# Optimization experiments

Hardware: AMD Instinct MI355X
Metric: run time of the kernel (lower is better)

Reference implementation:

```python
import jax, jax.numpy as jnp
import numpy as np

PRIOR = 0.2
TEMP = 1.0
THRESHOLD = 0.5
B, L, D, H = 8, 4096, 768, 512


def setup_inputs() -> dict:
    key = jax.random.key(0)
    k1, k2, k3, k4 = jax.random.split(key, 4)
    hidden = jax.random.normal(k1, (B, L, D), jnp.float32)
    # MLP params: Linear(D,H) -> ReLU -> Linear(H,1)
    W1 = jax.random.normal(k2, (D, H), jnp.float32) / np.sqrt(D).astype(np.float32)
    b1 = jnp.zeros((H,), jnp.float32)
    W2 = jax.random.normal(k3, (H, 1), jnp.float32) / np.sqrt(H).astype(np.float32)
    b2 = jnp.zeros((1,), jnp.float32)
    # pre-sampled uniform noise for the RelaxedBernoulli logistic reparameterization
    noise_u = jax.random.uniform(k4, (B, L), jnp.float32, minval=1e-6, maxval=1.0 - 1e-6)
    return dict(hidden=hidden, W1=W1, b1=b1, W2=W2, b2=b2, noise_u=noise_u)


def reference(hidden, W1, b1, W2, b2, noise_u):
    bs, seq_len, model_dim = hidden.shape
    # boundary MLP -> per-token logits [B, L]
    h = jax.nn.relu(jnp.einsum('bld,dh->blh', hidden, W1) + b1)
    logits = (jnp.einsum('blh,ho->blo', h, W2) + b2)[..., 0]
    # RelaxedBernoulli rsample: sigmoid((logits + logistic_noise) / temp),
    # since logit(sigmoid(logits)) == logits
    logistic_noise = jnp.log(noise_u) - jnp.log1p(-noise_u)
    soft_boundaries = jax.nn.sigmoid((logits + logistic_noise) / TEMP)
    hard_bin = (soft_boundaries > THRESHOLD).astype(soft_boundaries.dtype)
    # straight-through estimator
    hard_boundaries = soft_boundaries + jax.lax.stop_gradient(hard_bin - soft_boundaries)
    # segment id of each token: number of boundaries strictly before it
    # (boundary token is the last element of its segment)
    seg = (jnp.cumsum(hard_bin, axis=1) - hard_bin).astype(jnp.int32)  # [B, L] in [0, L)
    ids = (seg + seq_len * jnp.arange(bs, dtype=jnp.int32)[:, None]).reshape(-1)
    flat = hidden.reshape(bs * seq_len, model_dim)
    seg_sum = jax.ops.segment_sum(flat, ids, num_segments=bs * seq_len)
    seg_cnt = jax.ops.segment_sum(jnp.ones((bs * seq_len,), hidden.dtype), ids,
                                  num_segments=bs * seq_len)
    # mean pooling per segment; unused segment slots stay zero (padded to L segments,
    # equivalent to the torch [S,B,D]->transpose output up to zero padding)
    pooled = (seg_sum / jnp.maximum(seg_cnt, 1.0)[:, None]).reshape(bs, seq_len, model_dim)
    # hinge loss on boundary rate: penalize |rate - (prior+0.05)| beyond margin 0.05
    ratio = jnp.mean(hard_boundaries)
    loss = jax.nn.relu(jnp.abs(ratio - (PRIOR + 0.05)) - 0.05)
    num_boundaries = jnp.sum(hard_bin)
    total_positions = jnp.asarray(bs * seq_len, jnp.float32)
    return pooled, loss, num_boundaries, total_positions
```

## Files before the change

kernel.cpp:

```cpp
#include <hip/hip_runtime.h>
#include <math.h>

typedef __attribute__((ext_vector_type(8))) short short8;
typedef __attribute__((ext_vector_type(4))) float float4v;
typedef unsigned int uint;

#define BATCH 8
#define SEQ   4096
#define DIM   768
#define HID   512
#define M_TOK (BATCH * SEQ)

static __device__ __forceinline__ short f2bf_rne(float x) {
    unsigned int u = __float_as_uint(x);
    unsigned int r = (u + 0x7FFFu + ((u >> 16) & 1u)) >> 16;
    return (short)r;
}
static __device__ __forceinline__ uint pack_bf2(float a, float b) {
    return __builtin_amdgcn_perm(__float_as_uint(b), __float_as_uint(a), 0x07060302u);
}
union FragU { uint u[4]; short8 s; };

__global__ __launch_bounds__(256) void prep_kernel(const float* __restrict__ W1,
                                                   short* __restrict__ W1T) {
    int idx = blockIdx.x * 256 + threadIdx.x;
    if (idx < DIM * HID) {
        int k = idx / HID, n = idx % HID;
        W1T[n * DIM + k] = f2bf_rne(W1[idx]);
    }
}

__global__ __launch_bounds__(256) void mlp_kernel(const float* __restrict__ A,
                                                  const short* __restrict__ BT,
                                                  const float* __restrict__ b1,
                                                  const float* __restrict__ W2,
                                                  float* __restrict__ partial) {
    __shared__ short As[2][64 * 72];

    const int m0 = blockIdx.x * 64;
    const int tid = threadIdx.x;
    const int wave = tid >> 6, lane = tid & 63;
    const int quad = lane >> 4, r = lane & 15;
    const int srow = tid >> 2, scol = (tid & 3) * 16;
    const float* aPtr = A + (size_t)(m0 + srow) * DIM + scol;
    const int lw = srow * 72 + scol;
    const short* bPtr = BT + (size_t)(wave * 128 + r) * DIM + quad * 8;

    float4v s[4];
    short8  bfr[2][8];
#pragma unroll
    for (int i = 0; i < 4; i++) s[i] = *(const float4v*)(aPtr + i * 4);
#pragma unroll
    for (int j = 0; j < 8; j++) bfr[0][j] = *(const short8*)(bPtr + j * 16 * DIM);
    {
        uint pk[8];
#pragma unroll
        for (int i = 0; i < 4; i++) {
            pk[2 * i]     = pack_bf2(s[i][0], s[i][1]);
            pk[2 * i + 1] = pack_bf2(s[i][2], s[i][3]);
        }
        *(short8*)(&As[0][lw])     = *(short8*)&pk[0];
        *(short8*)(&As[0][lw + 8]) = *(short8*)&pk[4];
    }
    float4v acc[4][8] = {};
    __syncthreads();

    int ks = 0;
#pragma unroll
    for (int p = 0; p < 12; ++p) {
        const int cur = p & 1;
        if (p < 11) {
            const float* ap = aPtr + (p + 1) * 64;
#pragma unroll
            for (int i = 0; i < 4; i++) s[i] = *(const float4v*)(ap + i * 4);
        }
#pragma unroll
        for (int h = 0; h < 2; ++h, ++ks) {
            const int bb = ks & 1;
            if (ks < 23) {
                const short* bp = bPtr + (ks + 1) * 32;
#pragma unroll
                for (int j = 0; j < 8; j++)
                    bfr[bb ^ 1][j] = *(const short8*)(bp + j * 16 * DIM);
            }
            FragU af[4];
#pragma unroll
            for (int mf = 0; mf < 4; mf++)
                af[mf].s = *(const short8*)(&As[cur][(mf * 16 + r) * 72 + h * 32 + quad * 8]);
#pragma unroll
            for (int mf = 0; mf < 4; mf++)
#pragma unroll
                for (int j = 0; j < 8; j++)
                    acc[mf][j] = __builtin_amdgcn_mfma_f32_16x16x32_bf16(
                        af[mf].s, bfr[bb][j], acc[mf][j], 0, 0, 0);
        }
        if (p < 11) {
            uint pk[8];
#pragma unroll
            for (int i = 0; i < 4; i++) {
                pk[2 * i]     = pack_bf2(s[i][0], s[i][1]);
                pk[2 * i + 1] = pack_bf2(s[i][2], s[i][3]);
            }
            *(short8*)(&As[cur ^ 1][lw])     = *(short8*)&pk[0];
            *(short8*)(&As[cur ^ 1][lw + 8]) = *(short8*)&pk[4];
        }
        __syncthreads();
    }

    float b1v[8], w2v[8];
#pragma unroll
    for (int j = 0; j < 8; j++) {
        int gc = wave * 128 + j * 16 + r;
        b1v[j] = b1[gc];
        w2v[j] = W2[gc];
    }
#pragma unroll
    for (int mf = 0; mf < 4; mf++)
#pragma unroll
        for (int v = 0; v < 4; v++) {
            float pp = 0.f;
#pragma unroll
            for (int j = 0; j < 8; j++) {
                float hh = acc[mf][j][v] + b1v[j];
                hh = hh > 0.f ? hh : 0.f;
                pp += hh * w2v[j];
            }
#pragma unroll
            for (int off = 1; off < 16; off <<= 1) pp += __shfl_xor(pp, off, 64);
            if (r == 0)
                partial[(size_t)wave * M_TOK + m0 + mf * 16 + quad * 4 + v] = pp;
        }
}

__global__ __launch_bounds__(1024) void boundary_kernel(const float* __restrict__ partial,
                                                        const float* __restrict__ b2p,
                                                        const float* __restrict__ noise,
                                                        int* __restrict__ starts,
                                                        int* __restrict__ nseg,
                                                        int* __restrict__ nbcount) {
    const int b = blockIdx.x, tid = threadIdx.x;
    const int base = tid * 4;
    const float b2 = b2p[0];
    int h[4], c = 0;
#pragma unroll
    for (int j = 0; j < 4; j++) {
        int l = base + j;
        float u = noise[b * SEQ + l];
        float nz = logf(u) - log1pf(-u);
        float lg = b2 + nz;
#pragma unroll
        for (int q = 0; q < 4; q++) lg += partial[(size_t)q * M_TOK + b * SEQ + l];
        h[j] = (lg > 0.f) ? 1 : 0;
        c += h[j];
    }
    const int lane = tid & 63, wid = tid >> 6;
    int inc = c;
    for (int off = 1; off < 64; off <<= 1) {
        int t = __shfl_up(inc, off, 64);
        if (lane >= off) inc += t;
    }
    __shared__ int wtot[16], woff[16], extra[2];
    if (lane == 63) wtot[wid] = inc;
    if (tid == 1023) extra[0] = h[3];
    __syncthreads();
    if (tid == 0) {
        int s = 0;
        for (int i = 0; i < 16; i++) { woff[i] = s; s += wtot[i]; }
        extra[1] = s;
    }
    __syncthreads();
    int run = (inc - c) + woff[wid];
#pragma unroll
    for (int j = 0; j < 4; j++) {
        int l = base + j;
        if (h[j]) {
            run++;
            if (l < SEQ - 1) starts[b * (SEQ + 1) + run] = l + 1;
        }
    }
    if (tid == 0) {
        int total = extra[1];
        int ns = total + (extra[0] ? 0 : 1);
        starts[b * (SEQ + 1)] = 0;
        starts[b * (SEQ + 1) + ns] = SEQ;
        nseg[b] = ns;
        nbcount[b] = total;
    }
}

__global__ __launch_bounds__(256) void pool_kernel(const float* __restrict__ hidden,
                                                   const int* __restrict__ starts,
                                                   const int* __restrict__ nseg,
                                                   float* __restrict__ out) {
    const int wid = threadIdx.x >> 6, lane = threadIdx.x & 63;
    const int s = blockIdx.x * 4 + wid, b = blockIdx.y;
    float* orow = out + (size_t)(b * SEQ + s) * DIM;
    const int ns = nseg[b];
    if (s >= ns) {
        float4v z = {0.f, 0.f, 0.f, 0.f};
        *(float4v*)(orow + lane * 4)         = z;
        *(float4v*)(orow + (lane + 64) * 4)  = z;
        *(float4v*)(orow + (lane + 128) * 4) = z;
        return;
    }
    const int st = starts[b * (SEQ + 1) + s];
    const int en = starts[b * (SEQ + 1) + s + 1];
    float4v a0 = {0.f, 0.f, 0.f, 0.f}, a1 = a0, a2 = a0;
    const float* hbase = hidden + (size_t)(b * SEQ) * DIM;
    for (int row = st; row < en; row++) {
        const float* hr = hbase + (size_t)row * DIM;
        a0 += *(const float4v*)(hr + lane * 4);
        a1 += *(const float4v*)(hr + (lane + 64) * 4);
        a2 += *(const float4v*)(hr + (lane + 128) * 4);
    }
    const float invc = 1.f / (float)(en - st);
    a0 *= invc; a1 *= invc; a2 *= invc;
    *(float4v*)(orow + lane * 4)         = a0;
    *(float4v*)(orow + (lane + 64) * 4)  = a1;
    *(float4v*)(orow + (lane + 128) * 4) = a2;
}

__global__ void finalize_kernel(const int* __restrict__ nbcount, float* __restrict__ tail) {
    int nb = 0;
    for (int i = 0; i < BATCH; i++) nb += nbcount[i];
    float ratio = (float)nb / (float)M_TOK;
    float d = fabsf(ratio - 0.25f) - 0.05f;
    tail[0] = d > 0.f ? d : 0.f;
    tail[1] = (float)nb;
    tail[2] = (float)M_TOK;
}

extern "C" void kernel_launch(void* const* d_in, const int* in_sizes, int n_in,
                              void* d_out, int out_size, void* d_ws, size_t ws_size,
                              hipStream_t stream) {
    const float* hidden = (const float*)d_in[0];
    const float* W1     = (const float*)d_in[1];
    const float* b1     = (const float*)d_in[2];
    const float* W2     = (const float*)d_in[3];
    const float* b2     = (const float*)d_in[4];
    const float* noise  = (const float*)d_in[5];

    char* ws = (char*)d_ws;
    short* W1T     = (short*)(ws);
    float* partial = (float*)(ws + 786432);
    int*   starts  = (int*)(ws + 1310720);
    int*   nseg    = (int*)(ws + 1441824);
    int*   nbcount = nseg + 8;
    float* out     = (float*)d_out;

    prep_kernel<<<1536, 256, 0, stream>>>(W1, W1T);
    mlp_kernel<<<512, 256, 0, stream>>>(hidden, W1T, b1, W2, partial);
    boundary_kernel<<<BATCH, 1024, 0, stream>>>(partial, b2, noise, starts, nseg, nbcount);
    pool_kernel<<<dim3(SEQ / 4, BATCH), 256, 0, stream>>>(hidden, starts, nseg, out);
    finalize_kernel<<<1, 1, 0, stream>>>(nbcount, out + (size_t)M_TOK * DIM);
}
```

Measured before the change: 263.5 us.

## Stage GEMM operands via direct global-to-LDS loads and tile W1 transpose

The MLP GEMM now loads fp32 activations and bf16 weights straight into LDS with global_load_lds, using an XOR swizzle, and converts A to bf16 at fragment-read time instead of holding register-prefetched fragments. The four per-wave partial logits are reduced in shared memory, so one logits array is written instead of four. The W1 transpose uses a shared-memory tiled kernel with coalesced writes. The pool kernel unrolls its row loop by two and uses nontemporal stores. The GEMM loses its register double buffering and now syncs twice per 32-wide k-step, which could expose load latency.

```diff
diff --git a/kernel.cpp b/kernel.cpp
--- a/kernel.cpp
+++ b/kernel.cpp
@@ -20,119 +20,129 @@
     return __builtin_amdgcn_perm(__float_as_uint(b), __float_as_uint(a), 0x07060302u);
 }
 union FragU { uint u[4]; short8 s; };
+static __device__ __forceinline__ void gl2lds16(const void* g, void* l) {
+    __builtin_amdgcn_global_load_lds(
+        (const __attribute__((address_space(1))) unsigned int*)g,
+        (__attribute__((address_space(3))) unsigned int*)l, 16, 0, 0);
+}
 
 __global__ __launch_bounds__(256) void prep_kernel(const float* __restrict__ W1,
                                                    short* __restrict__ W1T) {
-    int idx = blockIdx.x * 256 + threadIdx.x;
-    if (idx < DIM * HID) {
-        int k = idx / HID, n = idx % HID;
-        W1T[n * DIM + k] = f2bf_rne(W1[idx]);
-    }
-}
-
-__global__ __launch_bounds__(256) void mlp_kernel(const float* __restrict__ A,
-                                                  const short* __restrict__ BT,
-                                                  const float* __restrict__ b1,
-                                                  const float* __restrict__ W2,
-                                                  float* __restrict__ partial) {
-    __shared__ short As[2][64 * 72];
+    __shared__ float t[64][65];
+    const int bk = blockIdx.x % 12, bn = blockIdx.x / 12;
+    const int k0 = bk * 64, n0 = bn * 64;
+    const int tr = threadIdx.x >> 6, tc = threadIdx.x & 63;
+#pragma unroll
+    for (int i = 0; i < 16; i++) {
+        int k = tr + i * 4;
+        t[k][tc] = W1[(size_t)(k0 + k) * HID + n0 + tc];
+    }
+    __syncthreads();
+#pragma unroll
+    for (int i = 0; i < 16; i++) {
+        int n = tr + i * 4;
+        W1T[(size_t)(n0 + n) * DIM + k0 + tc] = f2bf_rne(t[tc][n]);
+    }
+}
+
+#define AS_BYTES 8192
+#define BS_BYTES 32768
+__global__ __launch_bounds__(256, 2) void mlp_kernel(const float* __restrict__ A,
+                                                     const short* __restrict__ BT,
+                                                     const float* __restrict__ b1,
+                                                     const float* __restrict__ W2,
+                                                     float* __restrict__ logits) {
+    __shared__ float4v smem[(AS_BYTES + BS_BYTES) / 16];
+    char* Asb = (char*)smem;
+    char* Bsb = (char*)smem + AS_BYTES;
 
     const int m0 = blockIdx.x * 64;
-    const int tid = threadIdx.x;
-    const int wave = tid >> 6, lane = tid & 63;
+    const int tid = threadIdx.x, wave = tid >> 6, lane = tid & 63;
     const int quad = lane >> 4, r = lane & 15;
-    const int srow = tid >> 2, scol = (tid & 3) * 16;
-    const float* aPtr = A + (size_t)(m0 + srow) * DIM + scol;
-    const int lw = srow * 72 + scol;
-    const short* bPtr = BT + (size_t)(wave * 128 + r) * DIM + quad * 8;
-
-    float4v s[4];
-    short8  bfr[2][8];
-#pragma unroll
-    for (int i = 0; i < 4; i++) s[i] = *(const float4v*)(aPtr + i * 4);
-#pragma unroll
-    for (int j = 0; j < 8; j++) bfr[0][j] = *(const short8*)(bPtr + j * 16 * DIM);
-    {
-        uint pk[8];
-#pragma unroll
-        for (int i = 0; i < 4; i++) {
-            pk[2 * i]     = pack_bf2(s[i][0], s[i][1]);
-            pk[2 * i + 1] = pack_bf2(s[i][2], s[i][3]);
-        }
-        *(short8*)(&As[0][lw])     = *(short8*)&pk[0];
-        *(short8*)(&As[0][lw + 8]) = *(short8*)&pk[4];
-    }
+
+    int a_go[2], a_lds[2], b_go[8], b_lds[8];
+#pragma unroll
+    for (int j = 0; j < 2; j++) {
+        int ia = wave * 2 + j;
+        int row = ia * 8 + (lane >> 3);
+        int c = (lane & 7) ^ (row & 7);
+        a_go[j] = row * DIM + c * 4;
+        a_lds[j] = ia * 1024;
+    }
+#pragma unroll
+    for (int j = 0; j < 8; j++) {
+        int ib = wave * 8 + j;
+        int n = ib * 16 + (lane >> 2);
+        int c = lane & 3;
+        b_go[j] = n * DIM + c * 8;
+        b_lds[j] = ib * 1024;
+    }
+
     float4v acc[4][8] = {};
-    __syncthreads();
-
-    int ks = 0;
-#pragma unroll
-    for (int p = 0; p < 12; ++p) {
-        const int cur = p & 1;
-        if (p < 11) {
-            const float* ap = aPtr + (p + 1) * 64;
-#pragma unroll
-            for (int i = 0; i < 4; i++) s[i] = *(const float4v*)(ap + i * 4);
-        }
-#pragma unroll
-        for (int h = 0; h < 2; ++h, ++ks) {
-            const int bb = ks & 1;
-            if (ks < 23) {
-                const short* bp = bPtr + (ks + 1) * 32;
-#pragma unroll
-                for (int j = 0; j < 8; j++)
-                    bfr[bb ^ 1][j] = *(const short8*)(bp + j * 16 * DIM);
-            }
-            FragU af[4];
-#pragma unroll
-            for (int mf = 0; mf < 4; mf++)
-                af[mf].s = *(const short8*)(&As[cur][(mf * 16 + r) * 72 + h * 32 + quad * 8]);
-#pragma unroll
-            for (int mf = 0; mf < 4; mf++)
-#pragma unroll
-                for (int j = 0; j < 8; j++)
-                    acc[mf][j] = __builtin_amdgcn_mfma_f32_16x16x32_bf16(
-                        af[mf].s, bfr[bb][j], acc[mf][j], 0, 0, 0);
-        }
-        if (p < 11) {
-            uint pk[8];
-#pragma unroll
-            for (int i = 0; i < 4; i++) {
-                pk[2 * i]     = pack_bf2(s[i][0], s[i][1]);
-                pk[2 * i + 1] = pack_bf2(s[i][2], s[i][3]);
-            }
-            *(short8*)(&As[cur ^ 1][lw])     = *(short8*)&pk[0];
-            *(short8*)(&As[cur ^ 1][lw + 8]) = *(short8*)&pk[4];
-        }
+    const float* Abase = A + (size_t)m0 * DIM;
+
+    for (int p = 0; p < 24; ++p) {
+        const int k0 = p * 32;
+#pragma unroll
+        for (int j = 0; j < 2; j++) gl2lds16(Abase + a_go[j] + k0, Asb + a_lds[j]);
+#pragma unroll
+        for (int j = 0; j < 8; j++) gl2lds16(BT + b_go[j] + k0, Bsb + b_lds[j]);
         __syncthreads();
+
+        short8 bfr[8];
+#pragma unroll
+        for (int nf = 0; nf < 8; nf++)
+            bfr[nf] = *(const short8*)(Bsb + (wave * 128 + nf * 16 + r) * 64 + quad * 16);
+#pragma unroll
+        for (int mf = 0; mf < 4; mf++) {
+            int row = mf * 16 + r;
+            int e0 = (2 * quad) ^ (row & 7);
+            float4v f0 = *(const float4v*)(Asb + row * 128 + e0 * 16);
+            float4v f1 = *(const float4v*)(Asb + row * 128 + (e0 ^ 1) * 16);
+            FragU af;
+            af.u[0] = pack_bf2(f0[0], f0[1]);
+            af.u[1] = pack_bf2(f0[2], f0[3]);
+            af.u[2] = pack_bf2(f1[0], f1[1]);
+            af.u[3] = pack_bf2(f1[2], f1[3]);
+#pragma unroll
+            for (int nf = 0; nf < 8; nf++)
+                acc[mf][nf] = __builtin_amdgcn_mfma_f32_16x16x32_bf16(
+                    af.s, bfr[nf], acc[mf][nf], 0, 0, 0);
+        }
+        __syncthreads();
     }
 
     float b1v[8], w2v[8];
 #pragma unroll
-    for (int j = 0; j < 8; j++) {
-        int gc = wave * 128 + j * 16 + r;
-        b1v[j] = b1[gc];
-        w2v[j] = W2[gc];
-    }
+    for (int nf = 0; nf < 8; nf++) {
+        int gc = wave * 128 + nf * 16 + r;
+        b1v[nf] = b1[gc];
+        w2v[nf] = W2[gc];
+    }
+    float* red = (float*)Asb;
 #pragma unroll
     for (int mf = 0; mf < 4; mf++)
 #pragma unroll
         for (int v = 0; v < 4; v++) {
             float pp = 0.f;
 #pragma unroll
-            for (int j = 0; j < 8; j++) {
-                float hh = acc[mf][j][v] + b1v[j];
+            for (int nf = 0; nf < 8; nf++) {
+                float hh = acc[mf][nf][v] + b1v[nf];
                 hh = hh > 0.f ? hh : 0.f;
-                pp += hh * w2v[j];
+                pp += hh * w2v[nf];
             }
 #pragma unroll
             for (int off = 1; off < 16; off <<= 1) pp += __shfl_xor(pp, off, 64);
-            if (r == 0)
-                partial[(size_t)wave * M_TOK + m0 + mf * 16 + quad * 4 + v] = pp;
-        }
-}
-
-__global__ __launch_bounds__(1024) void boundary_kernel(const float* __restrict__ partial,
+            if (r == 0) red[wave * 64 + mf * 16 + quad * 4 + v] = pp;
+        }
+    __syncthreads();
+    if (tid < 64) {
+        float s = red[tid] + red[64 + tid] + red[128 + tid] + red[192 + tid];
+        logits[m0 + tid] = s;
+    }
+}
+
+__global__ __launch_bounds__(1024) void boundary_kernel(const float* __restrict__ logits,
                                                         const float* __restrict__ b2p,
                                                         const float* __restrict__ noise,
                                                         int* __restrict__ starts,
@@ -146,10 +156,7 @@
     for (int j = 0; j < 4; j++) {
         int l = base + j;
         float u = noise[b * SEQ + l];
-        float nz = logf(u) - log1pf(-u);
-        float lg = b2 + nz;
-#pragma unroll
-        for (int q = 0; q < 4; q++) lg += partial[(size_t)q * M_TOK + b * SEQ + l];
+        float lg = logits[b * SEQ + l] + b2 + logf(u) - log1pf(-u);
         h[j] = (lg > 0.f) ? 1 : 0;
         c += h[j];
     }
@@ -195,29 +202,37 @@
     const int wid = threadIdx.x >> 6, lane = threadIdx.x & 63;
     const int s = blockIdx.x * 4 + wid, b = blockIdx.y;
     float* orow = out + (size_t)(b * SEQ + s) * DIM;
+    float4v a0 = {0.f, 0.f, 0.f, 0.f}, a1 = a0, a2 = a0;
     const int ns = nseg[b];
-    if (s >= ns) {
-        float4v z = {0.f, 0.f, 0.f, 0.f};
-        *(float4v*)(orow + lane * 4)         = z;
-        *(float4v*)(orow + (lane + 64) * 4)  = z;
-        *(float4v*)(orow + (lane + 128) * 4) = z;
-        return;
-    }
-    const int st = starts[b * (SEQ + 1) + s];
-    const int en = starts[b * (SEQ + 1) + s + 1];
-    float4v a0 = {0.f, 0.f, 0.f, 0.f}, a1 = a0, a2 = a0;
-    const float* hbase = hidden + (size_t)(b * SEQ) * DIM;
-    for (int row = st; row < en; row++) {
-        const float* hr = hbase + (size_t)row * DIM;
-        a0 += *(const float4v*)(hr + lane * 4);
-        a1 += *(const float4v*)(hr + (lane + 64) * 4);
-        a2 += *(const float4v*)(hr + (lane + 128) * 4);
-    }
-    const float invc = 1.f / (float)(en - st);
-    a0 *= invc; a1 *= invc; a2 *= invc;
-    *(float4v*)(orow + lane * 4)         = a0;
-    *(float4v*)(orow + (lane + 64) * 4)  = a1;
-    *(float4v*)(orow + (lane + 128) * 4) = a2;
+    if (s < ns) {
+        const int st = starts[b * (SEQ + 1) + s];
+        const int en = starts[b * (SEQ + 1) + s + 1];
+        float4v c0 = a0, c1 = a0, c2 = a0;
+        const float* hbase = hidden + (size_t)(b * SEQ) * DIM;
+        int row = st;
+        for (; row + 2 <= en; row += 2) {
+            const float* h0 = hbase + (size_t)row * DIM;
+            const float* h1 = h0 + DIM;
+            a0 += *(const float4v*)(h0 + lane * 4);
+            a1 += *(const float4v*)(h0 + (lane + 64) * 4);
+            a2 += *(const float4v*)(h0 + (lane + 128) * 4);
+            c0 += *(const float4v*)(h1 + lane * 4);
+            c1 += *(const float4v*)(h1 + (lane + 64) * 4);
+            c2 += *(const float4v*)(h1 + (lane + 128) * 4);
+        }
+        if (row < en) {
+            const float* h0 = hbase + (size_t)row * DIM;
+            a0 += *(const float4v*)(h0 + lane * 4);
+            a1 += *(const float4v*)(h0 + (lane + 64) * 4);
+            a2 += *(const float4v*)(h0 + (lane + 128) * 4);
+        }
+        a0 += c0; a1 += c1; a2 += c2;
+        const float invc = 1.f / (float)(en - st);
+        a0 *= invc; a1 *= invc; a2 *= invc;
+    }
+    __builtin_nontemporal_store(a0, (float4v*)(orow + lane * 4));
+    __builtin_nontemporal_store(a1, (float4v*)(orow + (lane + 64) * 4));
+    __builtin_nontemporal_store(a2, (float4v*)(orow + (lane + 128) * 4));
 }
 
 __global__ void finalize_kernel(const int* __restrict__ nbcount, float* __restrict__ tail) {
@@ -241,16 +256,16 @@
     const float* noise  = (const float*)d_in[5];
 
     char* ws = (char*)d_ws;
-    short* W1T     = (short*)(ws);
-    float* partial = (float*)(ws + 786432);
-    int*   starts  = (int*)(ws + 1310720);
-    int*   nseg    = (int*)(ws + 1441824);
+    short* W1T    = (short*)(ws);
+    float* logits = (float*)(ws + 786432);
+    int*   starts = (int*)(ws + 917504);
+    int*   nseg   = (int*)(ws + 917504 + 131104);
     int*   nbcount = nseg + 8;
-    float* out     = (float*)d_out;
-
-    prep_kernel<<<1536, 256, 0, stream>>>(W1, W1T);
-    mlp_kernel<<<512, 256, 0, stream>>>(hidden, W1T, b1, W2, partial);
-    boundary_kernel<<<BATCH, 1024, 0, stream>>>(partial, b2, noise, starts, nseg, nbcount);
+    float* out    = (float*)d_out;
+
+    prep_kernel<<<96, 256, 0, stream>>>(W1, W1T);
+    mlp_kernel<<<512, 256, 0, stream>>>(hidden, W1T, b1, W2, logits);
+    boundary_kernel<<<BATCH, 1024, 0, stream>>>(logits, b2, noise, starts, nseg, nbcount);
     pool_kernel<<<dim3(SEQ / 4, BATCH), 256, 0, stream>>>(hidden, starts, nseg, out);
     finalize_kernel<<<1, 1, 0, stream>>>(nbcount, out + (size_t)M_TOK * DIM);
 }
```

New measurement: 242.5 us. -7.9%, faster.
